# Performance work log

Measured on AMD Instinct MI355X. Metric: run time of the kernel, lower is better.

## Reference

```python
import jax, jax.numpy as jnp
import numpy as np

N_HEADS = 8

def setup_inputs() -> dict:
    key = jax.random.key(0)
    ks = jax.random.split(key, 7)
    B, S, D = 4, 2048, 512
    s = 1.0 / np.sqrt(D)
    return {
        "input_Q": jax.random.normal(ks[0], (B, S, D), jnp.float32),
        "input_K": jax.random.normal(ks[1], (B, S, D), jnp.float32),
        "input_V": jax.random.normal(ks[2], (B, S, D), jnp.float32),
        "W_Q": jax.random.normal(ks[3], (D, D), jnp.float32) * s,
        "W_K": jax.random.normal(ks[4], (D, D), jnp.float32) * s,
        "W_V": jax.random.normal(ks[5], (D, D), jnp.float32) * s,
        "W_O": jax.random.normal(ks[6], (D, D), jnp.float32) * s,
    }

def reference(input_Q, input_K, input_V, W_Q, W_K, W_V, W_O):
    B, Sq, D = input_Q.shape
    Sk = input_K.shape[1]
    H = N_HEADS
    d_k = D // H
    # torch nn.Linear(bias=False): y = x @ W.T
    def proj(x, W):
        return (x @ W.T).reshape(B, -1, H, d_k).transpose(0, 2, 1, 3)  # [B,H,S,dk]
    Q = proj(input_Q, W_Q)
    K = proj(input_K, W_K)
    V = proj(input_V, W_V)
    scale = 1.0 / jnp.sqrt(jnp.float32(d_k))
    scores = jnp.einsum("bhqd,bhkd->bhqk", Q, K) * scale  # [B,H,Sq,Sk]
    # TriangularCausalMask: mask strict upper triangle with -inf
    causal = jnp.tril(jnp.ones((Sq, Sk), dtype=bool))
    scores = jnp.where(causal[None, None], scores, -jnp.inf)
    attn = jax.nn.softmax(scores, axis=-1)
    context = jnp.einsum("bhqk,bhkd->bhqd", attn, V)
    context = context.transpose(0, 2, 1, 3).reshape(B, Sq, D)
    return context @ W_O.T
```

## Files before the change

### kernel.cpp

```cpp
#include <hip/hip_runtime.h>
#include <hip/hip_bf16.h>
#include <math.h>

#define B_  4
#define S_  2048
#define D_  512
#define H_  8
#define DK_ 64
#define M_  (B_ * S_)

using bf16   = __bf16;
using bf16x4 = __bf16 __attribute__((ext_vector_type(4)));
using bf16x8 = __bf16 __attribute__((ext_vector_type(8)));
using f32x4  = float __attribute__((ext_vector_type(4)));

#define MFMA16(a, b, c) __builtin_amdgcn_mfma_f32_16x16x32_bf16((a), (b), (c), 0, 0, 0)
#define EXP2(x) exp2f(x)

typedef __attribute__((address_space(3))) void       lds_void;
typedef const __attribute__((address_space(1))) void gbl_void;

__device__ __forceinline__ void async16(const bf16* g, bf16* lds) {
    __builtin_amdgcn_global_load_lds((gbl_void*)g, (lds_void*)lds, 16, 0, 0);
}

__device__ __forceinline__ bf16x8 ldg8(const bf16* p) {
    return *reinterpret_cast<const bf16x8*>(p);
}

__device__ __forceinline__ size_t fragbase(int g, int k0, int kk, int t) {
    return ((((size_t)(g * 8 + k0) * 2 + kk) * 4 + t) * 64) * 8;
}

__global__ __launch_bounds__(256) void cvt_all(
    const float* __restrict__ x0, const float* __restrict__ x1, const float* __restrict__ x2,
    const float* __restrict__ w0, const float* __restrict__ w1,
    const float* __restrict__ w2, const float* __restrict__ w3,
    bf16* __restrict__ dst)
{
    const int w    = blockIdx.x * 4 + (threadIdx.x >> 6);
    const int lane = threadIdx.x & 63;
    const int lg = lane >> 4, lc = lane & 15;
    const float* src;
    int c;
    size_t dbase;
    if (w < 24576) {
        const int seg = w >> 13;
        c = w & 8191;
        src = (seg == 0) ? x0 : (seg == 1) ? x1 : x2;
        dbase = (size_t)seg << 22;
    } else {
        const int jj = w - 24576;
        const int seg = jj >> 9;
        c = jj & 511;
        src = (seg == 0) ? w0 : (seg == 1) ? w1 : (seg == 2) ? w2 : w3;
        dbase = ((size_t)3 << 22) + ((size_t)seg << 18);
    }
    const int g = c >> 6, k0 = (c >> 3) & 7, kk = (c >> 2) & 1, t = c & 3;
    const size_t soff = ((size_t)(g * 64 + t * 16 + lc) << 9) + k0 * 64 + kk * 32 + lg * 8;
    f32x4 a = *reinterpret_cast<const f32x4*>(src + soff);
    f32x4 b = *reinterpret_cast<const f32x4*>(src + soff + 4);
    bf16x8 r;
    #pragma unroll
    for (int j = 0; j < 4; ++j) { r[j] = (bf16)a[j]; r[j + 4] = (bf16)b[j]; }
    *reinterpret_cast<bf16x8*>(dst + dbase + ((size_t)c << 9) + (size_t)lane * 8) = r;
}

__global__ __launch_bounds__(256) void gemm_qkv(
    const bf16* __restrict__ Xf, const bf16* __restrict__ Wf,
    bf16* __restrict__ qkv)
{
    const int bx  = blockIdx.x;
    const int xcd = bx & 7;
    const int idx = bx >> 3;
    const int mt  = xcd + 8 * (idx & 7);
    const int rest = idx >> 3;
    const int nt  = rest & 3;
    const int z   = rest >> 2;

    const bf16* Xz = Xf + (size_t)z * M_ * D_;
    const bf16* Wz = Wf + (size_t)z * D_ * D_;
    const bool vz = (z == 2);
    const bf16* A  = vz ? Xz : Wz;
    const bf16* Bm = vz ? Wz : Xz;

    const int lane = threadIdx.x & 63;
    const int wave = threadIdx.x >> 6;
    const int lc = lane & 15;
    const int lg = lane >> 4;
    const int gAb = vz ? 2 * mt : 2 * nt;
    const int gBb = vz ? 2 * nt : 2 * mt;
    const int aIdx = wave >> 1;
    const int bIdx = wave & 1;
    const int gA = gAb + aIdx;
    const int gB = gBb + bIdx;

    __shared__ bf16 Ab[3][4096];
    __shared__ bf16 Bb[3][4096];

    auto stage = [&](int s) {
        const int k0 = s >> 1, kk = s & 1;
        bf16* ad = Ab[s % 3];
        bf16* bd = Bb[s % 3];
        #pragma unroll
        for (int i = 0; i < 4; ++i) {
            const int c  = wave * 4 + i;
            const int gx = (c >> 2) & 1;
            const int t  = c & 3;
            const bf16* srcb = (c < 8) ? A + fragbase(gAb + gx, k0, kk, t)
                                       : Bm + fragbase(gBb + gx, k0, kk, t);
            bf16* dstb = ((c < 8) ? ad : bd) + (gx * 4 + t) * 512;
            async16(srcb + (size_t)lane * 8, dstb + (size_t)lane * 8);
        }
    };

    f32x4 acc[4][4] = {};

    stage(0); stage(1);

    for (int s = 0; s < 16; ++s) {
        if (s + 1 < 16) asm volatile("s_waitcnt vmcnt(4)" ::: "memory");
        else            asm volatile("s_waitcnt vmcnt(0)" ::: "memory");
        __builtin_amdgcn_s_barrier();
        if (s + 2 < 16) stage(s + 2);

        const bf16* ab = Ab[s % 3] + aIdx * 2048;
        const bf16* bb = Bb[s % 3] + bIdx * 2048;
        bf16x8 af[4], bfm[4];
        #pragma unroll
        for (int t = 0; t < 4; ++t) {
            af[t]  = ldg8(ab + t * 512 + (size_t)lane * 8);
            bfm[t] = ldg8(bb + t * 512 + (size_t)lane * 8);
        }
        #pragma unroll
        for (int mi = 0; mi < 4; ++mi)
            #pragma unroll
            for (int ni = 0; ni < 4; ++ni)
                acc[mi][ni] = MFMA16(af[mi], bfm[ni], acc[mi][ni]);
    }

    if (z < 2) {
        bf16* Y = qkv + (size_t)z * M_ * D_;
        const float sc = (z == 0) ? 0.125f * 1.4426950408889634f : 1.0f;
        #pragma unroll
        for (int mi = 0; mi < 4; ++mi)
            #pragma unroll
            for (int ni = 0; ni < 4; ++ni) {
                const int d = gA * 64 + mi * 16 + lg * 4;
                const int s = gB * 64 + ni * 16 + lc;
                bf16x4 v;
                #pragma unroll
                for (int r = 0; r < 4; ++r) v[r] = (bf16)(acc[mi][ni][r] * sc);
                const size_t oidx =
                    ((((size_t)(s >> 11) * H_ + (d >> 6)) * S_
                      + (s & (S_ - 1))) << 6) + (d & 63);
                *reinterpret_cast<bf16x4*>(&Y[oidx]) = v;
            }
    } else {
        bf16* Y = qkv + (size_t)2 * M_ * D_;
        #pragma unroll
        for (int mi = 0; mi < 4; ++mi)
            #pragma unroll
            for (int ni = 0; ni < 4; ++ni) {
                const int s = gA * 64 + mi * 16 + lg * 4;
                const int d = gB * 64 + ni * 16 + lc;
                bf16x4 v;
                #pragma unroll
                for (int r = 0; r < 4; ++r) v[r] = (bf16)acc[mi][ni][r];
                const size_t oidx =
                    ((((size_t)(s >> 11)) * H_ + (d >> 6)) << 17)
                    + (size_t)(d & 63) * S_ + (s & (S_ - 1));
                *reinterpret_cast<bf16x4*>(&Y[oidx]) = v;
            }
    }
}

__global__ __launch_bounds__(256) void gemm_out(
    const bf16* __restrict__ CtxF, const bf16* __restrict__ WoF,
    float* __restrict__ out)
{
    const int bx  = blockIdx.x;
    const int xcd = bx & 7;
    const int idx = bx >> 3;
    const int mt  = xcd + 8 * (idx & 15);
    const int nt  = idx >> 4;

    const int lane = threadIdx.x & 63;
    const int wave = threadIdx.x >> 6;
    const int lc = lane & 15;
    const int lg = lane >> 4;
    const int gA = 2 * nt + (wave >> 1);
    const int tA = (wave & 1) * 2;
    const int gB = mt;

    __shared__ bf16 Ab[3][4096];
    __shared__ bf16 Bb[3][2048];

    auto stage = [&](int s) {
        const int k0 = s >> 1, kk = s & 1;
        bf16* ad = Ab[s % 3];
        bf16* bd = Bb[s % 3];
        #pragma unroll
        for (int i = 0; i < 3; ++i) {
            const int c = wave * 3 + i;
            if (c < 8) {
                const int gx = c >> 2, t = c & 3;
                async16(WoF + fragbase(2 * nt + gx, k0, kk, t) + (size_t)lane * 8,
                        ad + (gx * 4 + t) * 512 + (size_t)lane * 8);
            } else {
                const int t = c - 8;
                async16(CtxF + fragbase(gB, k0, kk, t) + (size_t)lane * 8,
                        bd + t * 512 + (size_t)lane * 8);
            }
        }
    };

    f32x4 acc[2][4] = {};

    stage(0); stage(1);

    for (int s = 0; s < 16; ++s) {
        if (s + 1 < 16) asm volatile("s_waitcnt vmcnt(3)" ::: "memory");
        else            asm volatile("s_waitcnt vmcnt(0)" ::: "memory");
        __builtin_amdgcn_s_barrier();
        if (s + 2 < 16) stage(s + 2);

        const bf16* ab = Ab[s % 3] + (wave >> 1) * 2048;
        const bf16* bb = Bb[s % 3];
        bf16x8 af[2], bfm[4];
        #pragma unroll
        for (int ai = 0; ai < 2; ++ai)
            af[ai] = ldg8(ab + (tA + ai) * 512 + (size_t)lane * 8);
        #pragma unroll
        for (int t = 0; t < 4; ++t)
            bfm[t] = ldg8(bb + t * 512 + (size_t)lane * 8);
        #pragma unroll
        for (int ai = 0; ai < 2; ++ai)
            #pragma unroll
            for (int ni = 0; ni < 4; ++ni)
                acc[ai][ni] = MFMA16(af[ai], bfm[ni], acc[ai][ni]);
    }

    #pragma unroll
    for (int ai = 0; ai < 2; ++ai)
        #pragma unroll
        for (int ni = 0; ni < 4; ++ni) {
            const int d = gA * 64 + (tA + ai) * 16 + lg * 4;
            const int s = gB * 64 + ni * 16 + lc;
            *reinterpret_cast<f32x4*>(&out[(size_t)s * D_ + d]) = acc[ai][ni];
        }
}

__device__ __forceinline__ bf16x8 pfrag(const f32x4 a, const f32x4 b) {
    union U4 { bf16x4 v; unsigned int u[2]; };
    U4 pa, pb;
    #pragma unroll
    for (int r = 0; r < 4; ++r) { pa.v[r] = (bf16)a[r]; pb.v[r] = (bf16)b[r]; }
    auto r0 = __builtin_amdgcn_permlane16_swap(pa.u[0], pb.u[0], false, false);
    auto r1 = __builtin_amdgcn_permlane16_swap(pa.u[1], pb.u[1], false, false);
    union U8 { unsigned int u[4]; bf16x8 v; } out;
    out.u[0] = r0[0]; out.u[1] = r1[0]; out.u[2] = r0[1]; out.u[3] = r1[1];
    return out.v;
}

__global__ __launch_bounds__(512, 4) void attn(
    const bf16* __restrict__ QKV, bf16* __restrict__ CtxF)
{
    const int bx = blockIdx.x;
    const int bh = (bx & 7) * 4 + ((bx >> 3) & 3);
    const int pi = bx >> 5;
    const int b = bh >> 3, h = bh & 7;
    const size_t plane = (size_t)S_ * DK_;
    const bf16* Q  = QKV + (size_t)bh * plane;
    const bf16* Kp = QKV + (size_t)(B_ * H_) * plane + (size_t)bh * plane;
    const bf16* Vt = QKV + 2 * (size_t)(B_ * H_) * plane + (size_t)bh * plane;

    const int lane = threadIdx.x & 63;
    const int wave = threadIdx.x >> 6;
    const int wv   = wave & 3;
    const int half = wave >> 2;
    const int lc = lane & 15;
    const int lg = lane >> 4;
    const int sg = ((lg & 1) << 1) | (lg >> 1);
    const int srow = wv * 16 + lc;
    const int mrow = wv * 16 + lc;

    __shared__ bf16 Ks[4][64 * 64];
    __shared__ bf16 Vs[4][64 * 64];

    const int lo = pi;
    const int hi = 31 - pi;
    const int myq = half ? lo : hi;

    const int qR = myq * 64 + mrow;
    bf16x8 qf0 = ldg8(Q + (size_t)qR * DK_ + lg * 8);
    bf16x8 qf1 = ldg8(Q + (size_t)qR * DK_ + 32 + lg * 8);

    f32x4 accO[4] = {};
    float li = 0.f;

    auto stage = [&](int n) {
        const int kn = n * 64;
        if (half == 0) {
            bf16* kd = Ks[n & 3];
            #pragma unroll
            for (int i = 0; i < 2; ++i) {
                const int kc = i * 4 + lg;
                async16(Kp + (size_t)(kn + srow) * DK_ + kc * 8,
                        kd + (i * 256 + wv * 64) * 8);
            }
        } else {
            bf16* vd = Vs[n & 3];
            #pragma unroll
            for (int i = 0; i < 2; ++i) {
                const int kcv = i * 4 + sg;
                async16(Vt + (size_t)srow * S_ + kn + kcv * 8,
                        vd + (i * 256 + wv * 64) * 8);
            }
        }
    };

    stage(0); stage(1); stage(2);

    for (int j = 0; j <= hi; ++j) {
        if (j + 2 <= hi)      asm volatile("s_waitcnt vmcnt(4)" ::: "memory");
        else if (j + 1 <= hi) asm volatile("s_waitcnt vmcnt(2)" ::: "memory");
        else                  asm volatile("s_waitcnt vmcnt(0)" ::: "memory");
        __builtin_amdgcn_s_barrier();
        if (j + 3 <= hi) stage(j + 3);

        if (j <= myq) {
            const bf16* ks = Ks[j & 3];
            const bf16* vs = Vs[j & 3];

            bf16x8 kf0[4], kf1[4], vf0[4], vf1[4];
            #pragma unroll
            for (int t = 0; t < 4; ++t) {
                kf0[t] = ldg8(&ks[(t * 64 + lane) * 8]);
                kf1[t] = ldg8(&ks[(256 + t * 64 + lane) * 8]);
                vf0[t] = ldg8(&vs[(t * 64 + lane) * 8]);
                vf1[t] = ldg8(&vs[(256 + t * 64 + lane) * 8]);
            }

            f32x4 st[4];
            #pragma unroll
            for (int t = 0; t < 4; ++t) {
                f32x4 zz = {};
                zz = MFMA16(kf0[t], qf0, zz);
                st[t] = MFMA16(kf1[t], qf1, zz);
            }
            float rs = 0.f;
            if (j == myq) {
                #pragma unroll
                for (int t = 0; t < 4; ++t)
                    #pragma unroll
                    for (int r = 0; r < 4; ++r) {
                        const int kl = t * 16 + lg * 4 + r;
                        const float pv = EXP2((kl <= mrow) ? st[t][r] : -1e30f);
                        st[t][r] = pv;
                        rs += pv;
                    }
            } else {
                #pragma unroll
                for (int t = 0; t < 4; ++t)
                    #pragma unroll
                    for (int r = 0; r < 4; ++r) {
                        const float pv = EXP2(st[t][r]);
                        st[t][r] = pv;
                        rs += pv;
                    }
            }
            li += rs;

            const bf16x8 p0 = pfrag(st[0], st[1]);
            const bf16x8 p1 = pfrag(st[2], st[3]);

            #pragma unroll
            for (int t = 0; t < 4; ++t) {
                accO[t] = MFMA16(vf0[t], p0, accO[t]);
                accO[t] = MFMA16(vf1[t], p1, accO[t]);
            }
        }
    }

    li += __shfl_xor(li, 16); li += __shfl_xor(li, 32);
    const float rl = 1.0f / li;
    __syncthreads();
    bf16* T = &Ks[0][0] + wave * 1280;

    #pragma unroll
    for (int t = 0; t < 4; ++t) {
        bf16x4 ov;
        #pragma unroll
        for (int r = 0; r < 4; ++r) ov[r] = (bf16)(accO[t][r] * rl);
        *reinterpret_cast<bf16x4*>(&T[lc * 72 + t * 16 + lg * 4]) = ov;
    }
    #pragma unroll
    for (int kk = 0; kk < 2; ++kk) {
        bf16x8 o8 = ldg8(&T[lc * 72 + kk * 32 + lg * 8]);
        *reinterpret_cast<bf16x8*>(
            &CtxF[fragbase(b * 32 + myq, h, kk, wv) + (size_t)lane * 8]) = o8;
    }
}

extern "C" void kernel_launch(void* const* d_in, const int* in_sizes, int n_in,
                              void* d_out, int out_size, void* d_ws, size_t ws_size,
                              hipStream_t stream)
{
    float* out = (float*)d_out;

    bf16* Xf   = (bf16*)d_ws;
    bf16* Wf   = Xf + (size_t)3 * M_ * D_;
    bf16* qkv  = Wf + (size_t)4 * D_ * D_;
    bf16* ctxF = qkv + (size_t)3 * M_ * D_;

    cvt_all<<<6656, 256, 0, stream>>>(
        (const float*)d_in[0], (const float*)d_in[1], (const float*)d_in[2],
        (const float*)d_in[3], (const float*)d_in[4], (const float*)d_in[5],
        (const float*)d_in[6], Xf);

    gemm_qkv<<<dim3(768), 256, 0, stream>>>(Xf, Wf, qkv);
    attn<<<dim3(512), 512, 0, stream>>>(qkv, ctxF);
    gemm_out<<<dim3(512), 256, 0, stream>>>(ctxF, Wf + (size_t)3 * D_ * D_, out);
}
```

Measured before the change: 174.8 us.

## Fuse fp32-to-bf16 activation conversion into QKV projection GEMM

The separate conversion pass over the Q/K/V activations is removed. The QKV GEMM now loads fp32 activations directly into registers, converts them to bf16 and writes the MFMA fragment layout into LDS, double-buffered with a register prefetch of the next stage. Weights are still converted once by a small kernel and loaded asynchronously into LDS. This saves the bf16 write and re-read of 3x8M activations, at the cost of register-staged loads in place of async LDS loads, a shallower two-stage pipeline, and each activation tile being converted by every N-tile block that reads it.

```diff
diff --git a/kernel.cpp b/kernel.cpp
--- a/kernel.cpp
+++ b/kernel.cpp
@@ -32,8 +32,7 @@
     return ((((size_t)(g * 8 + k0) * 2 + kk) * 4 + t) * 64) * 8;
 }
 
-__global__ __launch_bounds__(256) void cvt_all(
-    const float* __restrict__ x0, const float* __restrict__ x1, const float* __restrict__ x2,
+__global__ __launch_bounds__(256) void cvt_w(
     const float* __restrict__ w0, const float* __restrict__ w1,
     const float* __restrict__ w2, const float* __restrict__ w3,
     bf16* __restrict__ dst)
@@ -41,21 +40,10 @@
     const int w    = blockIdx.x * 4 + (threadIdx.x >> 6);
     const int lane = threadIdx.x & 63;
     const int lg = lane >> 4, lc = lane & 15;
-    const float* src;
-    int c;
-    size_t dbase;
-    if (w < 24576) {
-        const int seg = w >> 13;
-        c = w & 8191;
-        src = (seg == 0) ? x0 : (seg == 1) ? x1 : x2;
-        dbase = (size_t)seg << 22;
-    } else {
-        const int jj = w - 24576;
-        const int seg = jj >> 9;
-        c = jj & 511;
-        src = (seg == 0) ? w0 : (seg == 1) ? w1 : (seg == 2) ? w2 : w3;
-        dbase = ((size_t)3 << 22) + ((size_t)seg << 18);
-    }
+    const int seg = w >> 9;
+    const int c   = w & 511;
+    const float* src = (seg == 0) ? w0 : (seg == 1) ? w1 : (seg == 2) ? w2 : w3;
+    const size_t dbase = (size_t)seg << 18;
     const int g = c >> 6, k0 = (c >> 3) & 7, kk = (c >> 2) & 1, t = c & 3;
     const size_t soff = ((size_t)(g * 64 + t * 16 + lc) << 9) + k0 * 64 + kk * 32 + lg * 8;
     f32x4 a = *reinterpret_cast<const f32x4*>(src + soff);
@@ -66,8 +54,9 @@
     *reinterpret_cast<bf16x8*>(dst + dbase + ((size_t)c << 9) + (size_t)lane * 8) = r;
 }
 
-__global__ __launch_bounds__(256) void gemm_qkv(
-    const bf16* __restrict__ Xf, const bf16* __restrict__ Wf,
+__global__ __launch_bounds__(256, 3) void gemm_qkv(
+    const float* __restrict__ x0, const float* __restrict__ x1,
+    const float* __restrict__ x2, const bf16* __restrict__ Wf,
     bf16* __restrict__ qkv)
 {
     const int bx  = blockIdx.x;
@@ -78,66 +67,94 @@
     const int nt  = rest & 3;
     const int z   = rest >> 2;
 
-    const bf16* Xz = Xf + (size_t)z * M_ * D_;
-    const bf16* Wz = Wf + (size_t)z * D_ * D_;
+    const float* X  = (z == 0) ? x0 : (z == 1) ? x1 : x2;
+    const bf16*  Wz = Wf + (size_t)z * D_ * D_;
     const bool vz = (z == 2);
-    const bf16* A  = vz ? Xz : Wz;
-    const bf16* Bm = vz ? Wz : Xz;
 
     const int lane = threadIdx.x & 63;
     const int wave = threadIdx.x >> 6;
     const int lc = lane & 15;
     const int lg = lane >> 4;
-    const int gAb = vz ? 2 * mt : 2 * nt;
-    const int gBb = vz ? 2 * nt : 2 * mt;
     const int aIdx = wave >> 1;
     const int bIdx = wave & 1;
-    const int gA = gAb + aIdx;
-    const int gB = gBb + bIdx;
-
-    __shared__ bf16 Ab[3][4096];
-    __shared__ bf16 Bb[3][4096];
-
-    auto stage = [&](int s) {
+
+    __shared__ bf16 Wb[2][4096];
+    __shared__ bf16 Xb[2][4096];
+
+    const int tid  = threadIdx.x;
+    const int xc   = tid >> 5;
+    const int xgx  = xc >> 2, xt = xc & 3;
+    const int sub  = tid & 31;
+    const int l0   = 2 * sub;
+    const int xrow0 = (2 * mt + xgx) * 64 + xt * 16 + (l0 & 15);
+    const int xcolg = (l0 >> 4) * 8;
+
+    auto issueX = [&](int s, f32x4* r) {
+        const int col = (s >> 1) * 64 + (s & 1) * 32 + xcolg;
+        const float* p0 = X + (size_t)xrow0 * 512 + col;
+        r[0] = *reinterpret_cast<const f32x4*>(p0);
+        r[1] = *reinterpret_cast<const f32x4*>(p0 + 4);
+        r[2] = *reinterpret_cast<const f32x4*>(p0 + 512);
+        r[3] = *reinterpret_cast<const f32x4*>(p0 + 516);
+    };
+    auto issueW = [&](int s) {
         const int k0 = s >> 1, kk = s & 1;
-        bf16* ad = Ab[s % 3];
-        bf16* bd = Bb[s % 3];
-        #pragma unroll
-        for (int i = 0; i < 4; ++i) {
-            const int c  = wave * 4 + i;
-            const int gx = (c >> 2) & 1;
-            const int t  = c & 3;
-            const bf16* srcb = (c < 8) ? A + fragbase(gAb + gx, k0, kk, t)
-                                       : Bm + fragbase(gBb + gx, k0, kk, t);
-            bf16* dstb = ((c < 8) ? ad : bd) + (gx * 4 + t) * 512;
-            async16(srcb + (size_t)lane * 8, dstb + (size_t)lane * 8);
+        bf16* wd = Wb[s & 1];
+        #pragma unroll
+        for (int i = 0; i < 2; ++i) {
+            const int c = wave * 2 + i;
+            const int gx = c >> 2, t = c & 3;
+            async16(Wz + fragbase(2 * nt + gx, k0, kk, t) + (size_t)lane * 8,
+                    wd + (gx * 4 + t) * 512 + (size_t)lane * 8);
         }
     };
+    auto writeX = [&](int s, const f32x4* r) {
+        bf16* xd = Xb[s & 1];
+        bf16x8 v0, v1;
+        #pragma unroll
+        for (int j = 0; j < 4; ++j) {
+            v0[j] = (bf16)r[0][j]; v0[j + 4] = (bf16)r[1][j];
+            v1[j] = (bf16)r[2][j]; v1[j + 4] = (bf16)r[3][j];
+        }
+        *reinterpret_cast<bf16x8*>(xd + xc * 512 + l0 * 8)       = v0;
+        *reinterpret_cast<bf16x8*>(xd + xc * 512 + (l0 + 1) * 8) = v1;
+    };
 
     f32x4 acc[4][4] = {};
 
-    stage(0); stage(1);
+    {
+        f32x4 xr[4];
+        issueX(0, xr); issueW(0);
+        writeX(0, xr);
+        __syncthreads();
+    }
 
     for (int s = 0; s < 16; ++s) {
-        if (s + 1 < 16) asm volatile("s_waitcnt vmcnt(4)" ::: "memory");
-        else            asm volatile("s_waitcnt vmcnt(0)" ::: "memory");
-        __builtin_amdgcn_s_barrier();
-        if (s + 2 < 16) stage(s + 2);
-
-        const bf16* ab = Ab[s % 3] + aIdx * 2048;
-        const bf16* bb = Bb[s % 3] + bIdx * 2048;
+        f32x4 xn[4];
+        if (s < 15) { issueX(s + 1, xn); issueW(s + 1); }
+
+        const bf16* wb = Wb[s & 1];
+        const bf16* xb = Xb[s & 1];
+        const bf16* ap = (vz ? xb : wb) + aIdx * 2048;
+        const bf16* bp = (vz ? wb : xb) + bIdx * 2048;
         bf16x8 af[4], bfm[4];
         #pragma unroll
         for (int t = 0; t < 4; ++t) {
-            af[t]  = ldg8(ab + t * 512 + (size_t)lane * 8);
-            bfm[t] = ldg8(bb + t * 512 + (size_t)lane * 8);
+            af[t]  = ldg8(ap + t * 512 + (size_t)lane * 8);
+            bfm[t] = ldg8(bp + t * 512 + (size_t)lane * 8);
         }
         #pragma unroll
         for (int mi = 0; mi < 4; ++mi)
             #pragma unroll
             for (int ni = 0; ni < 4; ++ni)
                 acc[mi][ni] = MFMA16(af[mi], bfm[ni], acc[mi][ni]);
-    }
+
+        if (s < 15) writeX(s + 1, xn);
+        __syncthreads();
+    }
+
+    const int gA = (vz ? 2 * mt : 2 * nt) + aIdx;
+    const int gB = (vz ? 2 * nt : 2 * mt) + bIdx;
 
     if (z < 2) {
         bf16* Y = qkv + (size_t)z * M_ * D_;
@@ -409,17 +426,18 @@
 {
     float* out = (float*)d_out;
 
-    bf16* Xf   = (bf16*)d_ws;
-    bf16* Wf   = Xf + (size_t)3 * M_ * D_;
+    bf16* Wf   = (bf16*)d_ws;
     bf16* qkv  = Wf + (size_t)4 * D_ * D_;
     bf16* ctxF = qkv + (size_t)3 * M_ * D_;
 
-    cvt_all<<<6656, 256, 0, stream>>>(
+    cvt_w<<<512, 256, 0, stream>>>(
+        (const float*)d_in[3], (const float*)d_in[4],
+        (const float*)d_in[5], (const float*)d_in[6], Wf);
+
+    gemm_qkv<<<dim3(768), 256, 0, stream>>>(
         (const float*)d_in[0], (const float*)d_in[1], (const float*)d_in[2],
-        (const float*)d_in[3], (const float*)d_in[4], (const float*)d_in[5],
-        (const float*)d_in[6], Xf);
-
-    gemm_qkv<<<dim3(768), 256, 0, stream>>>(Xf, Wf, qkv);
+        Wf, qkv);
+
     attn<<<dim3(512), 512, 0, stream>>>(qkv, ctxF);
     gemm_out<<<dim3(512), 256, 0, stream>>>(ctxF, Wf + (size_t)3 * D_ * D_, out);
 }
```

Measured after the change: 181.9 us. 4.1% more time.
